# Performance work log

Hardware: AMD Instinct MI355X
Metric: run time of the kernel (lower is better)

Reference implementation:

```python
import jax, jax.numpy as jnp
import numpy as np

B, N, D, K = 2048, 65536, 256, 32
TEMP = 0.1  # config.temperature
EPS = 1e-4  # constant from -log(1 - sim + 0.0001)


def setup_inputs() -> dict:
    key = jax.random.key(0)
    k1, k2, k3, k4 = jax.random.split(key, 4)
    x = jax.random.normal(k1, (B, D), jnp.float32)
    x = x / jnp.linalg.norm(x, axis=-1, keepdims=True)  # unit-sphere latents
    mu = jax.random.normal(k2, (N, D), jnp.float32)
    mu = mu / jnp.linalg.norm(mu, axis=-1, keepdims=True)  # splat centers on sphere
    alpha = jax.random.uniform(k3, (N,), jnp.float32, 0.5, 2.0)  # splat sharpness > 0
    W = jax.random.normal(k4, (1, 3), jnp.float32) * 0.5  # W_comp: Linear(3,1)
    b = jnp.zeros((1,), jnp.float32)
    return {"x": x, "mu": mu, "alpha": alpha, "W": W, "b": b, "knn_k": K}


def reference(x, mu, alpha, W, b, knn_k):
    # --- kNN over splat store by dot-product similarity ---
    sims = x @ mu.T                               # [B, N]
    vals, idx = jax.lax.top_k(sims, knn_k)        # [B, K]; vals == bmm(neighbors_mu, x)

    # --- E_splats(x) = -logsumexp(alpha_k * (x.mu_k - 1) / tau) ---
    a = alpha[idx]                                # [B, K] gathered neighbor alphas
    exponent = a * (vals - 1.0) / TEMP
    e_splat = -jax.nn.logsumexp(exponent, axis=-1)  # [B]

    # --- E_geom: mean over off-diagonal pairs of -log(1 - x_i.x_j + eps) ---
    bs = x @ x.T                                  # [B, B]
    Bn = x.shape[0]
    offdiag = ~jnp.eye(Bn, dtype=bool)
    terms = -jnp.log(1.0 - bs + EPS)
    e_geom = jnp.sum(jnp.where(offdiag, terms, 0.0)) / (Bn * (Bn - 1))

    # --- E_comp: sigmoid(W.[u, v, u*v] + b) with u, v = top-2 neighbor dots ---
    u = vals[:, 0:1]                              # [B, 1]
    v = vals[:, 1:2]                              # [B, 1]
    uv = jnp.concatenate([u, v, u * v], axis=-1)  # [B, 3]
    e_comp = jax.nn.sigmoid(uv @ W.T + b)[:, 0]   # [B]

    return e_splat + 0.01 * e_geom + 0.05 * e_comp
```

## Files before the change

kernel.cpp:

```cpp
#include <hip/hip_runtime.h>
#include <hip/hip_bf16.h>
#include <math.h>

#define BDIM 2048
#define NDIM 65536
#define DDIM 256
#define KTOP 32
#define TEMP_INV 10.0f
#define EPS_GEOM 1e-4f

#define TSEL  0.18f
#define TSEL8 0.17f
#define CAP 512
#define KPL (CAP / 64)
#define REFINE 64

#define SCRN_BLOCKS ((BDIM / 128) * (NDIM / 128))
#define EG_BLOCKS   ((BDIM / 128) * (BDIM / 128))
#define XP_BLOCKS   (BDIM * DDIM / 2048)
#define MP_BLOCKS   (NDIM * DDIM / 2048)
#define MUF_BLOCKS  (NDIM / 16)
#define XF_BLOCKS   (BDIM / 16)

typedef unsigned long long u64;
typedef __attribute__((ext_vector_type(8))) short bf16x8;
typedef __attribute__((ext_vector_type(4))) float f32x4;

#define GLD16(gptr, lptr)                                                     \
  __builtin_amdgcn_global_load_lds(                                           \
      (const __attribute__((address_space(1))) void*)(gptr),                  \
      (__attribute__((address_space(3))) void*)(lptr), 16, 0, 0)

__device__ __forceinline__ float bflo(unsigned u) { return __uint_as_float(u << 16); }
__device__ __forceinline__ float bfhi(unsigned u) { return __uint_as_float(u & 0xffff0000u); }

__device__ __forceinline__ float loadInput(const void* p, int i, int isf32) {
  if (isf32) return ((const float*)p)[i];
  return __uint_as_float(((unsigned)((const unsigned short*)p)[i]) << 16);
}

__device__ __forceinline__ short f2bf(float f) {
  const unsigned u = __float_as_uint(f);
  return (short)((u + 0x7fffu + ((u >> 16) & 1u)) >> 16);
}

__device__ __forceinline__ void load8f(const void* p, size_t i, int isf32, float* f) {
  if (isf32) {
    const float* gp = (const float*)p + i;
    const float4 a = *(const float4*)gp;
    const float4 b = *(const float4*)(gp + 4);
    f[0] = a.x; f[1] = a.y; f[2] = a.z; f[3] = a.w;
    f[4] = b.x; f[5] = b.y; f[6] = b.z; f[7] = b.w;
  } else {
    const uint4 q = *(const uint4*)((const unsigned short*)p + i);
    f[0] = bflo(q.x); f[1] = bfhi(q.x); f[2] = bflo(q.y); f[3] = bfhi(q.y);
    f[4] = bflo(q.z); f[5] = bfhi(q.z); f[6] = bflo(q.w); f[7] = bfhi(q.w);
  }
}

__device__ __forceinline__ uint2 pk8fp8(const float* f) {
  int w0 = 0, w1 = 0;
  w0 = __builtin_amdgcn_cvt_pk_fp8_f32(f[0], f[1], w0, false);
  w0 = __builtin_amdgcn_cvt_pk_fp8_f32(f[2], f[3], w0, true);
  w1 = __builtin_amdgcn_cvt_pk_fp8_f32(f[4], f[5], w1, false);
  w1 = __builtin_amdgcn_cvt_pk_fp8_f32(f[6], f[7], w1, true);
  uint2 r; r.x = (unsigned)w0; r.y = (unsigned)w1; return r;
}

__device__ __forceinline__ long long mk64(unsigned lo, unsigned hi) {
  return (long long)(((u64)hi << 32) | (u64)lo);
}

__device__ __forceinline__ unsigned packCand(float sim, int col) {
  return (((unsigned)(unsigned short)f2bf(sim)) << 16) | (0xFFFFu - (unsigned)col);
}

__device__ __forceinline__ unsigned enc32(float f) {
  const unsigned u = __float_as_uint(f);
  return u ^ ((u & 0x80000000u) ? 0xFFFFFFFFu : 0x80000000u);
}
__device__ __forceinline__ float dec32(unsigned c) {
  const unsigned u = (c & 0x80000000u) ? (c ^ 0x80000000u) : ~c;
  return __uint_as_float(u);
}

__global__ __launch_bounds__(256)
void detect_init_kernel(const void* __restrict__ x, const void* __restrict__ mu,
                        const void* __restrict__ alpha, const void* __restrict__ W,
                        int* __restrict__ flags, float* __restrict__ egeom,
                        int* __restrict__ cnt) {
  const int tid = threadIdx.x;
  for (int i = tid; i < BDIM; i += 256) cnt[i] = 0;
  if (tid == 0) *egeom = 0.f;

  const int t = tid >> 6, lane = tid & 63;
  const void* ptrs[4] = { x, mu, alpha, W };
  const int   nel[4]  = { BDIM * DDIM, NDIM * DDIM, NDIM, 3 };
  const unsigned* p = (const unsigned*)ptrs[t];
  int nw = nel[t] / 2;
  if (nw > 2048) nw = 2048;
  int sane = 0, tot = 0;
  for (int i = lane; i < nw; i += 64) {
    const unsigned lo = p[i] & 0xffffu;
    const int eb = (int)((lo >> 7) & 0xffu);
    sane += (lo == 0u || (eb >= 96 && eb <= 160)) ? 1 : 0;
    tot  += 1;
  }
  #pragma unroll
  for (int off = 1; off < 64; off <<= 1) {
    sane += __shfl_xor(sane, off);
    tot  += __shfl_xor(tot, off);
  }
  if (lane == 0) flags[t] = (2 * sane < tot) ? 1 : 0;
}

__global__ __launch_bounds__(256)
void prep_kernel(const void* __restrict__ x, const void* __restrict__ mu,
                 const int* __restrict__ flags,
                 unsigned short* __restrict__ xb, unsigned short* __restrict__ mub,
                 unsigned char* __restrict__ x8f, unsigned char* __restrict__ mu8f,
                 const int use_fp8, const int use_mub) {
  const int bx = blockIdx.x;
  const int tid = threadIdx.x;
  if (bx < XP_BLOCKS) {
    const size_t i = ((size_t)bx * 256 + tid) * 8;
    float f[8];
    load8f(x, i, flags[0], f);
    bf16x8 v;
    #pragma unroll
    for (int j = 0; j < 8; ++j) v[j] = f2bf(f[j]);
    *(bf16x8*)(xb + i) = v;
    return;
  }
  if (use_fp8) {
    __shared__ float sm[16][257];
    const bool isx = (bx >= XP_BLOCKS + MUF_BLOCKS);
    const int rg = isx ? (bx - XP_BLOCKS - MUF_BLOCKS) : (bx - XP_BLOCKS);
    const void* src = isx ? x : mu;
    const int isf32 = isx ? flags[0] : flags[1];
    unsigned char* dst = (isx ? x8f : mu8f) + (size_t)rg * 4096;
    if (isf32) {
      const float* s32 = (const float*)src + (size_t)rg * 16 * DDIM;
      #pragma unroll
      for (int q = 0; q < 4; ++q) {
        const int idx = q * 256 + tid;
        const int r = idx >> 6, c4 = (idx & 63) * 4;
        const float4 v = *(const float4*)(s32 + (size_t)r * DDIM + c4);
        sm[r][c4] = v.x; sm[r][c4 + 1] = v.y; sm[r][c4 + 2] = v.z; sm[r][c4 + 3] = v.w;
      }
    } else {
      #pragma unroll
      for (int q = 0; q < 2; ++q) {
        const int idx = q * 256 + tid;
        const int r = idx >> 5, c8 = (idx & 31) * 8;
        float f[8];
        load8f(src, (size_t)(rg * 16 + r) * DDIM + c8, 0, f);
        #pragma unroll
        for (int j = 0; j < 8; ++j) sm[r][c8 + j] = f[j];
      }
    }
    __syncthreads();
    const int p = tid >> 6, L = tid & 63;
    const int r = L & 15, c0 = p * 64 + ((L >> 4) & 3) * 8;
    float f0[8], f1[8];
    #pragma unroll
    for (int j = 0; j < 8; ++j) { f0[j] = sm[r][c0 + j]; f1[j] = sm[r][c0 + 32 + j]; }
    const uint2 lo = pk8fp8(f0), hi = pk8fp8(f1);
    uint4 o; o.x = lo.x; o.y = lo.y; o.z = hi.x; o.w = hi.y;
    *(uint4*)(dst + (size_t)p * 1024 + (size_t)L * 16) = o;
  } else {
    if (!use_mub || !flags[1]) return;
    const size_t i = (((size_t)(bx - XP_BLOCKS)) * 256 + tid) * 8;
    float f[8];
    load8f(mu, i, 1, f);
    bf16x8 v;
    #pragma unroll
    for (int j = 0; j < 8; ++j) v[j] = f2bf(f[j]);
    *(bf16x8*)(mub + i) = v;
  }
}

__global__ __launch_bounds__(256, 3)
void gemm_fp8_kernel(const unsigned char* __restrict__ x8f,
                     const unsigned char* __restrict__ mu8f,
                     int* __restrict__ cnt, int* __restrict__ cidx,
                     float* __restrict__ accum) {
  __shared__ float red[4];
  const int tid = threadIdx.x;
  const int w = tid >> 6, L = tid & 63;
  const int rw = w >> 1, cw = w & 1;
  const int midx = L & 15;

  const int h = blockIdx.x;
  const bool is_eg = (h >= SCRN_BLOCKS);
  int row0, col0;
  const unsigned char* bsrc;
  if (is_eg) {
    const int eb = h - SCRN_BLOCKS;
    row0 = (eb >> 4) * 128;
    col0 = (eb & 15) * 128;
    bsrc = x8f;
  } else {
    const int lid = (h & 7) * 1024 + (h >> 3);
    row0 = (lid & 15) * 128;
    col0 = (lid >> 4) * 128;
    bsrc = mu8f;
  }

  const unsigned char* ab = x8f + ((size_t)((row0 >> 4) + rw * 4)) * 4096 + (size_t)L * 16;
  const unsigned char* bb = bsrc + ((size_t)((col0 >> 4) + cw * 4)) * 4096 + (size_t)L * 16;

  f32x4 acc[4][4];
  #pragma unroll
  for (int g = 0; g < 4; ++g)
    #pragma unroll
    for (int c = 0; c < 4; ++c)
      acc[g][c] = (f32x4){0.f, 0.f, 0.f, 0.f};

  #pragma unroll
  for (int p = 0; p < 4; ++p) {
    uint4 av[4], bv[4];
    #pragma unroll
    for (int g = 0; g < 4; ++g)
      av[g] = *(const uint4*)(ab + (size_t)g * 4096 + (size_t)p * 1024);
    #pragma unroll
    for (int c = 0; c < 4; ++c)
      bv[c] = *(const uint4*)(bb + (size_t)c * 4096 + (size_t)p * 1024);
    #pragma unroll
    for (int g = 0; g < 4; ++g)
      #pragma unroll
      for (int c = 0; c < 4; ++c) {
        acc[g][c] = __builtin_amdgcn_mfma_f32_16x16x32_fp8_fp8(
            mk64(av[g].x, av[g].y), mk64(bv[c].x, bv[c].y), acc[g][c], 0, 0, 0);
        acc[g][c] = __builtin_amdgcn_mfma_f32_16x16x32_fp8_fp8(
            mk64(av[g].z, av[g].w), mk64(bv[c].z, bv[c].w), acc[g][c], 0, 0, 0);
      }
  }

  const int quad4 = (L >> 4) * 4;
  if (!is_eg) {
    #pragma unroll
    for (int g = 0; g < 4; ++g) {
      const int rowb = row0 + rw * 64 + g * 16 + quad4;
      #pragma unroll
      for (int c = 0; c < 4; ++c) {
        const int col = col0 + cw * 64 + c * 16 + midx;
        #pragma unroll
        for (int t = 0; t < 4; ++t) {
          if (acc[g][c][t] >= TSEL8) {
            const int row = rowb + t;
            const int pos = atomicAdd(&cnt[row], 1);
            if (pos < CAP) cidx[row * CAP + pos] = (int)packCand(acc[g][c][t], col);
          }
        }
      }
    }
  } else {
    float local = 0.f;
    #pragma unroll
    for (int g = 0; g < 4; ++g) {
      const int rowb = row0 + rw * 64 + g * 16 + quad4;
      #pragma unroll
      for (int c = 0; c < 4; ++c) {
        const int col = col0 + cw * 64 + c * 16 + midx;
        #pragma unroll
        for (int t = 0; t < 4; ++t) {
          if (rowb + t != col) {
            float arg = 1.0f - acc[g][c][t] + EPS_GEOM;
            arg = fmaxf(arg, 1e-20f);
            local += -logf(arg);
          }
        }
      }
    }
    #pragma unroll
    for (int off = 1; off < 64; off <<= 1) local += __shfl_xor(local, off);
    if (L == 0) red[w] = local;
    __syncthreads();
    if (tid == 0) atomicAdd(accum, red[0] + red[1] + red[2] + red[3]);
  }
}

__global__ __launch_bounds__(256, 3)
void gemm_bf16_kernel(const unsigned short* __restrict__ xb, const void* __restrict__ mu,
                      const unsigned short* __restrict__ mub, const int use_mub,
                      const int* __restrict__ flags,
                      int* __restrict__ cnt, int* __restrict__ cidx,
                      float* __restrict__ accum) {
  __shared__ __align__(16) unsigned char As[2][8 * 1024];
  __shared__ __align__(16) unsigned char Bs[2][8 * 1024];
  __shared__ float red[4];
  const int tid = threadIdx.x;
  const int w = tid >> 6, L = tid & 63;
  const int midx = L & 15;
  const int koff = (L >> 4) * 8;
  const int rw = w >> 1, cw = w & 1;

  const int h = blockIdx.x;
  const bool is_eg = (h >= SCRN_BLOCKS);
  int row0, col0, bfast;
  const unsigned short* bs16;
  if (is_eg) {
    const int eb = h - SCRN_BLOCKS;
    col0 = (eb & 15) * 128;
    row0 = (eb >> 4) * 128;
    bs16 = xb;
    bfast = 1;
  } else {
    const int lid = (h & 7) * 1024 + (h >> 3);
    row0 = (lid & 15) * 128;
    col0 = (lid >> 4) * 128;
    const int isf32m = flags[1];
    bs16 = isf32m ? mub : (const unsigned short*)mu;
    bfast = (!isf32m) || use_mub;
  }

  f32x4 acc[4][4];
  #pragma unroll
  for (int g = 0; g < 4; ++g)
    #pragma unroll
    for (int c = 0; c < 4; ++c)
      acc[g][c] = (f32x4){0.f, 0.f, 0.f, 0.f};

  auto stage = [&](int kc, int buf) {
    #pragma unroll
    for (int q = 0; q < 4; ++q) {
      const int t = w * 4 + q;
      if (t < 8) {
        const size_t ge = (size_t)(row0 + t * 16 + midx) * DDIM + kc + koff;
        GLD16(xb + ge, As[buf] + (size_t)t * 1024);
      } else {
        const int hb = t - 8;
        const size_t ge = (size_t)(col0 + hb * 16 + midx) * DDIM + kc + koff;
        if (bfast) {
          GLD16(bs16 + ge, Bs[buf] + (size_t)hb * 1024);
        } else {
          const float* gp = (const float*)mu + ge;
          const float4 f0 = *(const float4*)gp;
          const float4 f1 = *(const float4*)(gp + 4);
          bf16x8 v;
          v[0] = f2bf(f0.x); v[1] = f2bf(f0.y); v[2] = f2bf(f0.z); v[3] = f2bf(f0.w);
          v[4] = f2bf(f1.x); v[5] = f2bf(f1.y); v[6] = f2bf(f1.z); v[7] = f2bf(f1.w);
          *((bf16x8*)(Bs[buf] + (size_t)hb * 1024 + (size_t)L * 16)) = v;
        }
      }
    }
  };

  stage(0, 0);
  __syncthreads();
  int cur = 0;
  for (int kc = 32; kc <= DDIM; kc += 32) {
    if (kc < DDIM) stage(kc, cur ^ 1);
    bf16x8 af[4], bfr[4];
    #pragma unroll
    for (int g = 0; g < 4; ++g)
      af[g] = *(const bf16x8*)(As[cur] + (size_t)(rw * 4 + g) * 1024 + (size_t)L * 16);
    #pragma unroll
    for (int c = 0; c < 4; ++c)
      bfr[c] = *(const bf16x8*)(Bs[cur] + (size_t)(cw * 4 + c) * 1024 + (size_t)L * 16);
    #pragma unroll
    for (int g = 0; g < 4; ++g)
      #pragma unroll
      for (int c = 0; c < 4; ++c)
        acc[g][c] = __builtin_amdgcn_mfma_f32_16x16x32_bf16(af[g], bfr[c], acc[g][c], 0, 0, 0);
    __syncthreads();
    cur ^= 1;
  }

  const int quad4 = (L >> 4) * 4;
  if (!is_eg) {
    #pragma unroll
    for (int g = 0; g < 4; ++g) {
      const int rowb = row0 + rw * 64 + g * 16 + quad4;
      #pragma unroll
      for (int c = 0; c < 4; ++c) {
        const int col = col0 + cw * 64 + c * 16 + midx;
        #pragma unroll
        for (int t = 0; t < 4; ++t) {
          if (acc[g][c][t] >= TSEL) {
            const int row = rowb + t;
            const int pos = atomicAdd(&cnt[row], 1);
            if (pos < CAP) cidx[row * CAP + pos] = (int)packCand(acc[g][c][t], col);
          }
        }
      }
    }
  } else {
    float local = 0.f;
    #pragma unroll
    for (int g = 0; g < 4; ++g) {
      const int rowb = row0 + rw * 64 + g * 16 + quad4;
      #pragma unroll
      for (int c = 0; c < 4; ++c) {
        const int col = col0 + cw * 64 + c * 16 + midx;
        #pragma unroll
        for (int t = 0; t < 4; ++t) {
          if (rowb + t != col) {
            float arg = 1.0f - acc[g][c][t] + EPS_GEOM;
            arg = fmaxf(arg, 1e-20f);
            local += -logf(arg);
          }
        }
      }
    }
    #pragma unroll
    for (int off = 1; off < 64; off <<= 1) local += __shfl_xor(local, off);
    if (L == 0) red[w] = local;
    __syncthreads();
    if (tid == 0) atomicAdd(accum, red[0] + red[1] + red[2] + red[3]);
  }
}

__global__ __launch_bounds__(256)
void final_kernel(const int* __restrict__ cnt, const int* __restrict__ cidx,
                  const void* __restrict__ x, const void* __restrict__ mu,
                  const void* __restrict__ alpha, const void* __restrict__ W,
                  const void* __restrict__ bptr, const float* __restrict__ egeom,
                  const int* __restrict__ flags, float* __restrict__ out) {
  __shared__ float xrow[DDIM];
  __shared__ int   scol[CAP];
  __shared__ float cv[CAP];
  __shared__ float tv[KTOP];
  __shared__ int   tix[KTOP];
  __shared__ int   selcnt;
  const int tid = threadIdx.x;
  const int w = tid >> 6, L = tid & 63;
  const int half = L >> 5, hl = L & 31;
  const int row = blockIdx.x;
  const int isf32x = flags[0], isf32m = flags[1];
  const int isf32a = flags[2], isf32w = flags[3];
  int n = cnt[row]; if (n > CAP) n = CAP;
  if (tid == 0) selcnt = 0;

  for (int i = tid; i < DDIM; i += 256)
    xrow[i] = loadInput(x, row * DDIM + i, isf32x);
  __syncthreads();

  if (w == 0) {
    unsigned ent[KPL], v16[KPL];
    #pragma unroll
    for (int j = 0; j < KPL; ++j) {
      const int sidx = j * 64 + L;
      ent[j] = (sidx < n) ? (unsigned)cidx[row * CAP + sidx] : 0u;
      v16[j] = ent[j] >> 16;
    }
    unsigned T = 0;
    if (n > REFINE) {
      for (int bit = 15; bit >= 0; --bit) {
        const unsigned candT = T | (1u << bit);
        int c = 0;
        #pragma unroll
        for (int j = 0; j < KPL; ++j) c += (v16[j] >= candT) ? 1 : 0;
        #pragma unroll
        for (int off = 1; off < 64; off <<= 1) c += __shfl_xor(c, off);
        if (c >= REFINE) T = candT;
      }
    }
    #pragma unroll
    for (int j = 0; j < KPL; ++j) {
      if (ent[j] != 0u && v16[j] >= T) {
        const int p = atomicAdd(&selcnt, 1);
        scol[p] = (int)(0xFFFFu - (ent[j] & 0xFFFFu));
      }
    }
  }
  __syncthreads();
  const int m = selcnt;

  float x8r[8];
  #pragma unroll
  for (int j = 0; j < 8; ++j) x8r[j] = xrow[hl * 8 + j];

  for (int base = w * 2; base < m; base += 8) {
    const int cno = base + half;
    float s = 0.f;
    if (cno < m) {
      const int col = scol[cno];
      const size_t e = (size_t)col * DDIM + hl * 8;
      float m8[8];
      if (isf32m) {
        const float* gp = (const float*)mu + e;
        const float4 f0 = *(const float4*)gp;
        const float4 f1 = *(const float4*)(gp + 4);
        m8[0] = f0.x; m8[1] = f0.y; m8[2] = f0.z; m8[3] = f0.w;
        m8[4] = f1.x; m8[5] = f1.y; m8[6] = f1.z; m8[7] = f1.w;
      } else {
        const uint4 q = *(const uint4*)((const unsigned short*)mu + e);
        m8[0] = bflo(q.x); m8[1] = bfhi(q.x); m8[2] = bflo(q.y); m8[3] = bfhi(q.y);
        m8[4] = bflo(q.z); m8[5] = bfhi(q.z); m8[6] = bflo(q.w); m8[7] = bfhi(q.w);
      }
      #pragma unroll
      for (int j = 0; j < 8; ++j) s += x8r[j] * m8[j];
    }
    #pragma unroll
    for (int off = 1; off < 32; off <<= 1) s += __shfl_xor(s, off);
    if (hl == 0 && cno < m) cv[cno] = s;
  }
  __syncthreads();
  if (tid >= 64) return;

  u64 key[KPL];
  #pragma unroll
  for (int j = 0; j < KPL; ++j) {
    const int sidx = j * 64 + L;
    key[j] = 0;
    if (sidx < m)
      key[j] = ((u64)enc32(cv[sidx]) << 32) |
               (u64)(0xFFFFFFFFu - (unsigned)scol[sidx]);
  }
  for (int round = 0; round < KTOP; ++round) {
    u64 lm = key[0];
    #pragma unroll
    for (int j = 1; j < KPL; ++j) lm = (key[j] > lm) ? key[j] : lm;
    u64 wm = lm;
    #pragma unroll
    for (int off = 1; off < 64; off <<= 1) {
      const unsigned lo = __shfl_xor((unsigned)wm, off);
      const unsigned hi = __shfl_xor((unsigned)(wm >> 32), off);
      const u64 o = ((u64)hi << 32) | lo;
      wm = (o > wm) ? o : wm;
    }
    #pragma unroll
    for (int j = 0; j < KPL; ++j) if (key[j] == wm) key[j] = 0;
    if (L == 0) {
      if (wm != 0) {
        tv[round]  = dec32((unsigned)(wm >> 32));
        tix[round] = (int)(0xFFFFFFFFu - (unsigned)(wm & 0xFFFFFFFFu));
      } else { tv[round] = 0.f; tix[round] = 0; }
    }
  }

  float e = -1e30f;
  if (L < KTOP) {
    const float a = loadInput(alpha, tix[L], isf32a);
    e = a * (tv[L] - 1.0f) * TEMP_INV;
  }
  float mx = e;
  #pragma unroll
  for (int off = 1; off < 64; off <<= 1) mx = fmaxf(mx, __shfl_xor(mx, off));
  float p = (L < KTOP) ? expf(e - mx) : 0.f;
  #pragma unroll
  for (int off = 1; off < 64; off <<= 1) p += __shfl_xor(p, off);

  if (L == 0) {
    const float e_splat = -(mx + logf(p));
    const float uu = tv[0], vv = tv[1];
    const float W0 = loadInput(W, 0, isf32w), W1 = loadInput(W, 1, isf32w);
    const float W2 = loadInput(W, 2, isf32w), b0 = loadInput(bptr, 0, isf32w);
    const float z = W0 * uu + W1 * vv + W2 * uu * vv + b0;
    const float e_comp = 1.0f / (1.0f + expf(-z));
    const float eg = egeom[0] * (1.0f / ((float)BDIM * (float)(BDIM - 1)));
    out[row] = e_splat + 0.01f * eg + 0.05f * e_comp;
  }
}

extern "C" void kernel_launch(void* const* d_in, const int* in_sizes, int n_in,
                              void* d_out, int out_size, void* d_ws, size_t ws_size,
                              hipStream_t stream) {
  const void* x     = d_in[0];
  const void* mu    = d_in[1];
  const void* alpha = d_in[2];
  const void* W     = d_in[3];
  const void* b     = d_in[4];

  char* ws = (char*)d_ws;
  int*            flags = (int*)ws;
  float*          egeom = (float*)(ws + 64);
  int*            cnt   = (int*)(ws + 256);
  int*            cidx  = (int*)(ws + 8448);
  unsigned short* xb    = (unsigned short*)(ws + 8448 + (size_t)BDIM * CAP * 4);
  const size_t    AUX_OFF = 8448 + (size_t)BDIM * CAP * 4 + (size_t)BDIM * DDIM * 2;
  const size_t    X8_BYTES  = (size_t)BDIM * DDIM;
  const size_t    MU8_BYTES = (size_t)NDIM * DDIM;
  const int       use_fp8 = (ws_size >= AUX_OFF + X8_BYTES + MU8_BYTES) ? 1 : 0;
  unsigned char*  x8f   = (unsigned char*)(ws + AUX_OFF);
  unsigned char*  mu8f  = (unsigned char*)(ws + AUX_OFF + X8_BYTES);
  const size_t    MUB_BYTES = (size_t)NDIM * DDIM * 2;
  const int       use_mub = (!use_fp8 && ws_size >= AUX_OFF + MUB_BYTES) ? 1 : 0;
  unsigned short* mub   = (unsigned short*)(ws + (use_mub ? AUX_OFF : 0));
  float*          out   = (float*)d_out;

  detect_init_kernel<<<1, 256, 0, stream>>>(x, mu, alpha, W, flags, egeom, cnt);
  const int nprep = XP_BLOCKS + (use_fp8 ? (MUF_BLOCKS + XF_BLOCKS)
                                         : (use_mub ? MP_BLOCKS : 0));
  prep_kernel<<<nprep, 256, 0, stream>>>(
      x, mu, flags, xb, mub, x8f, mu8f, use_fp8, use_mub);
  if (use_fp8) {
    gemm_fp8_kernel<<<SCRN_BLOCKS + EG_BLOCKS, 256, 0, stream>>>(
        x8f, mu8f, cnt, cidx, egeom);
  } else {
    gemm_bf16_kernel<<<SCRN_BLOCKS + EG_BLOCKS, 256, 0, stream>>>(
        xb, mu, mub, use_mub, flags, cnt, cidx, egeom);
  }
  final_kernel<<<BDIM, 256, 0, stream>>>(cnt, cidx, x, mu, alpha, W, b, egeom, flags, out);
}
```

Measured before the change: 274.8 us.

## Reuse fp8 A fragments across four column tiles per block; trim top-k loops

Each block of the fp8 screening GEMM now keeps its x fragments in registers and walks four consecutive 128-column tiles of mu, so the grid shrinks by a factor of four and x reloads drop accordingly. The egeom reduction is accumulated across the tiles before a single atomic per block. In the final kernel, the top-k key loops run only over the populated candidate slots (jmax) rather than the full fixed KPL. Holding the A fragments adds register pressure, and the variable-bound key loops may force key[] out of registers into scratch.

```diff
diff --git a/kernel.cpp b/kernel.cpp
--- a/kernel.cpp
+++ b/kernel.cpp
@@ -14,6 +14,10 @@
 #define CAP 512
 #define KPL (CAP / 64)
 #define REFINE 64
+
+#define NTF8 4
+#define SCRN_F8 ((BDIM / 128) * (NDIM / (128 * NTF8)))
+#define EG_F8   ((BDIM / 128) * (BDIM / (128 * NTF8)))
 
 #define SCRN_BLOCKS ((BDIM / 128) * (NDIM / 128))
 #define EG_BLOCKS   ((BDIM / 128) * (BDIM / 128))
@@ -192,90 +196,102 @@
   const int midx = L & 15;
 
   const int h = blockIdx.x;
-  const bool is_eg = (h >= SCRN_BLOCKS);
-  int row0, col0;
+  const bool is_eg = (h >= SCRN_F8);
+  int row0, colbase;
   const unsigned char* bsrc;
   if (is_eg) {
-    const int eb = h - SCRN_BLOCKS;
-    row0 = (eb >> 4) * 128;
-    col0 = (eb & 15) * 128;
+    const int eb = h - SCRN_F8;
+    row0 = (eb >> 2) * 128;
+    colbase = (eb & 3) * (128 * NTF8);
     bsrc = x8f;
   } else {
-    const int lid = (h & 7) * 1024 + (h >> 3);
+    const int lid = (h & 7) * 256 + (h >> 3);
     row0 = (lid & 15) * 128;
-    col0 = (lid >> 4) * 128;
+    colbase = (lid >> 4) * (128 * NTF8);
     bsrc = mu8f;
   }
 
   const unsigned char* ab = x8f + ((size_t)((row0 >> 4) + rw * 4)) * 4096 + (size_t)L * 16;
-  const unsigned char* bb = bsrc + ((size_t)((col0 >> 4) + cw * 4)) * 4096 + (size_t)L * 16;
-
-  f32x4 acc[4][4];
+  uint4 af[4][4];
   #pragma unroll
-  for (int g = 0; g < 4; ++g)
-    #pragma unroll
-    for (int c = 0; c < 4; ++c)
-      acc[g][c] = (f32x4){0.f, 0.f, 0.f, 0.f};
-
-  #pragma unroll
-  for (int p = 0; p < 4; ++p) {
-    uint4 av[4], bv[4];
+  for (int p = 0; p < 4; ++p)
     #pragma unroll
     for (int g = 0; g < 4; ++g)
-      av[g] = *(const uint4*)(ab + (size_t)g * 4096 + (size_t)p * 1024);
-    #pragma unroll
-    for (int c = 0; c < 4; ++c)
-      bv[c] = *(const uint4*)(bb + (size_t)c * 4096 + (size_t)p * 1024);
+      af[p][g] = *(const uint4*)(ab + (size_t)g * 4096 + (size_t)p * 1024);
+
+  const int quad4 = (L >> 4) * 4;
+  float eg_local = 0.f;
+
+  #pragma unroll 1
+  for (int ct = 0; ct < NTF8; ++ct) {
+    const int col0 = colbase + ct * 128;
+    const unsigned char* bb = bsrc + ((size_t)((col0 >> 4) + cw * 4)) * 4096 + (size_t)L * 16;
+
+    f32x4 acc[4][4];
     #pragma unroll
     for (int g = 0; g < 4; ++g)
       #pragma unroll
-      for (int c = 0; c < 4; ++c) {
-        acc[g][c] = __builtin_amdgcn_mfma_f32_16x16x32_fp8_fp8(
-            mk64(av[g].x, av[g].y), mk64(bv[c].x, bv[c].y), acc[g][c], 0, 0, 0);
-        acc[g][c] = __builtin_amdgcn_mfma_f32_16x16x32_fp8_fp8(
-            mk64(av[g].z, av[g].w), mk64(bv[c].z, bv[c].w), acc[g][c], 0, 0, 0);
-      }
-  }
-
-  const int quad4 = (L >> 4) * 4;
-  if (!is_eg) {
-    #pragma unroll
-    for (int g = 0; g < 4; ++g) {
-      const int rowb = row0 + rw * 64 + g * 16 + quad4;
-      #pragma unroll
-      for (int c = 0; c < 4; ++c) {
-        const int col = col0 + cw * 64 + c * 16 + midx;
-        #pragma unroll
-        for (int t = 0; t < 4; ++t) {
-          if (acc[g][c][t] >= TSEL8) {
-            const int row = rowb + t;
-            const int pos = atomicAdd(&cnt[row], 1);
-            if (pos < CAP) cidx[row * CAP + pos] = (int)packCand(acc[g][c][t], col);
+      for (int c = 0; c < 4; ++c)
+        acc[g][c] = (f32x4){0.f, 0.f, 0.f, 0.f};
+
+    #pragma unroll
+    for (int p = 0; p < 4; ++p) {
+      uint4 bv[4];
+      #pragma unroll
+      for (int c = 0; c < 4; ++c)
+        bv[c] = *(const uint4*)(bb + (size_t)c * 4096 + (size_t)p * 1024);
+      #pragma unroll
+      for (int g = 0; g < 4; ++g)
+        #pragma unroll
+        for (int c = 0; c < 4; ++c) {
+          acc[g][c] = __builtin_amdgcn_mfma_f32_16x16x32_fp8_fp8(
+              mk64(af[p][g].x, af[p][g].y), mk64(bv[c].x, bv[c].y), acc[g][c], 0, 0, 0);
+          acc[g][c] = __builtin_amdgcn_mfma_f32_16x16x32_fp8_fp8(
+              mk64(af[p][g].z, af[p][g].w), mk64(bv[c].z, bv[c].w), acc[g][c], 0, 0, 0);
+        }
+    }
+
+    if (!is_eg) {
+      #pragma unroll
+      for (int g = 0; g < 4; ++g) {
+        const int rowb = row0 + rw * 64 + g * 16 + quad4;
+        #pragma unroll
+        for (int c = 0; c < 4; ++c) {
+          const int col = col0 + cw * 64 + c * 16 + midx;
+          #pragma unroll
+          for (int t = 0; t < 4; ++t) {
+            if (acc[g][c][t] >= TSEL8) {
+              const int row = rowb + t;
+              const int pos = atomicAdd(&cnt[row], 1);
+              if (pos < CAP) cidx[row * CAP + pos] = (int)packCand(acc[g][c][t], col);
+            }
           }
         }
       }
-    }
-  } else {
-    float local = 0.f;
-    #pragma unroll
-    for (int g = 0; g < 4; ++g) {
-      const int rowb = row0 + rw * 64 + g * 16 + quad4;
-      #pragma unroll
-      for (int c = 0; c < 4; ++c) {
-        const int col = col0 + cw * 64 + c * 16 + midx;
-        #pragma unroll
-        for (int t = 0; t < 4; ++t) {
-          if (rowb + t != col) {
-            float arg = 1.0f - acc[g][c][t] + EPS_GEOM;
-            arg = fmaxf(arg, 1e-20f);
-            local += -logf(arg);
+    } else {
+      #pragma unroll
+      for (int g = 0; g < 4; ++g) {
+        const int rowb = row0 + rw * 64 + g * 16 + quad4;
+        #pragma unroll
+        for (int c = 0; c < 4; ++c) {
+          const int col = col0 + cw * 64 + c * 16 + midx;
+          #pragma unroll
+          for (int t = 0; t < 4; ++t) {
+            if (rowb + t != col) {
+              float arg = 1.0f - acc[g][c][t] + EPS_GEOM;
+              arg = fmaxf(arg, 1e-20f);
+              eg_local += -logf(arg);
+            }
           }
         }
       }
     }
-    #pragma unroll
-    for (int off = 1; off < 64; off <<= 1) local += __shfl_xor(local, off);
-    if (L == 0) red[w] = local;
+  }
+
+  if (is_eg) {
+    #pragma unroll
+    for (int off = 1; off < 64; off <<= 1) eg_local += __shfl_xor(eg_local, off);
+    if (L == 0) red[w] = eg_local;
     __syncthreads();
     if (tid == 0) atomicAdd(accum, red[0] + red[1] + red[2] + red[3]);
   }
@@ -500,9 +516,9 @@
   __syncthreads();
   if (tid >= 64) return;
 
+  const int jmax = (m + 63) >> 6;
   u64 key[KPL];
-  #pragma unroll
-  for (int j = 0; j < KPL; ++j) {
+  for (int j = 0; j < jmax; ++j) {
     const int sidx = j * 64 + L;
     key[j] = 0;
     if (sidx < m)
@@ -510,9 +526,8 @@
                (u64)(0xFFFFFFFFu - (unsigned)scol[sidx]);
   }
   for (int round = 0; round < KTOP; ++round) {
-    u64 lm = key[0];
-    #pragma unroll
-    for (int j = 1; j < KPL; ++j) lm = (key[j] > lm) ? key[j] : lm;
+    u64 lm = 0;
+    for (int j = 0; j < jmax; ++j) lm = (key[j] > lm) ? key[j] : lm;
     u64 wm = lm;
     #pragma unroll
     for (int off = 1; off < 64; off <<= 1) {
@@ -521,8 +536,7 @@
       const u64 o = ((u64)hi << 32) | lo;
       wm = (o > wm) ? o : wm;
     }
-    #pragma unroll
-    for (int j = 0; j < KPL; ++j) if (key[j] == wm) key[j] = 0;
+    for (int j = 0; j < jmax; ++j) if (key[j] == wm) key[j] = 0;
     if (L == 0) {
       if (wm != 0) {
         tv[round]  = dec32((unsigned)(wm >> 32));
@@ -587,7 +601,7 @@
   prep_kernel<<<nprep, 256, 0, stream>>>(
       x, mu, flags, xb, mub, x8f, mu8f, use_fp8, use_mub);
   if (use_fp8) {
-    gemm_fp8_kernel<<<SCRN_BLOCKS + EG_BLOCKS, 256, 0, stream>>>(
+    gemm_fp8_kernel<<<SCRN_F8 + EG_F8, 256, 0, stream>>>(
         x8f, mu8f, cnt, cidx, egeom);
   } else {
     gemm_bf16_kernel<<<SCRN_BLOCKS + EG_BLOCKS, 256, 0, stream>>>(
```

After: 336.2 us. 1.22x slower.
